# Performance work log

Hardware: AMD Instinct MI355X
Metric: run time of the kernel (lower is better)

Reference implementation:

```python
import jax, jax.numpy as jnp
import numpy as np

TAU = 0.95

def _f1_per_position(labels):
    # labels: [B, L] binary relevance. r[b, j] = F1 if the list is truncated at position j+1.
    B, L = labels.shape
    csum = jnp.cumsum(labels, axis=1)                       # [B, L] relevant docs kept at cutoff k=j+1
    k = jnp.arange(1, L + 1, dtype=labels.dtype)            # [L]
    total = jnp.sum(labels, axis=1, keepdims=True)          # [B, 1] total relevant per list
    prec = csum / k
    rec = jnp.where(total > 0, csum / jnp.maximum(total, 1.0), 0.0)
    denom = prec + rec
    return jnp.where(denom > 0, 2.0 * prec * rec / jnp.maximum(denom, 1e-20), 0.0)


def setup_inputs() -> dict:
    key = jax.random.key(0)
    k1, k2 = jax.random.split(key)
    B, L = 8192, 2048
    # output: per-position truncation probabilities in (0, 1); log() is applied in the loss.
    output = jax.random.uniform(k1, (B, L, 1), dtype=jnp.float32, minval=1e-4, maxval=1.0)
    labels = jax.random.randint(k2, (B, L), 0, 2).astype(jnp.float32)
    return {"output": output, "labels": labels}


def reference(output, labels):
    # output: [B, L, 1], labels: [B, L]
    B = output.shape[0]
    r = _f1_per_position(labels)                             # [B, L]
    # q = exp(r/tau) / sum_j exp(r/tau)  ==  softmax(r/tau) along positions
    q = jax.nn.softmax(r / TAU, axis=1)
    log_out = jnp.log(output[..., 0])                        # [B, L]
    return -jnp.sum(log_out * q) / B
```

## Files before the change

### kernel.cpp

```cpp
#include <hip/hip_runtime.h>


constexpr int L   = 2048;
constexpr int TPB = 256;
constexpr float TAU   = 0.95f;
constexpr float LOG2E = 1.4426950408889634f;
constexpr float LN2   = 0.6931471805599453f;

__global__ __launch_bounds__(TPB) void attncut_row_kernel(
    const float* __restrict__ output,
    const float* __restrict__ labels,
    float* __restrict__ rowloss,
    int B)
{
    const int wave = threadIdx.x >> 6;
    const int lane = threadIdx.x & 63;
    const int row  = blockIdx.x * 4 + wave;

    const float4* lab4 = reinterpret_cast<const float4*>(labels + (size_t)row * L) + lane;
    const float4* out4 = reinterpret_cast<const float4*>(output + (size_t)row * L) + lane;

    float4 lb[8], ov[8];
#pragma unroll
    for (int c = 0; c < 8; ++c) lb[c] = lab4[c * 64];
#pragma unroll
    for (int c = 0; c < 8; ++c) ov[c] = out4[c * 64];

    unsigned nibs = 0u;
#pragma unroll
    for (int c = 0; c < 8; ++c) {
        float4 a = lb[c];
        unsigned b = (unsigned)a.x | ((unsigned)a.y << 1)
                   | ((unsigned)a.z << 2) | ((unsigned)a.w << 3);
        nibs |= b << (4 * c);
    }

    unsigned w[4];
#pragma unroll
    for (int q = 0; q < 4; ++q) {
        unsigned c0 = __popc((nibs >> (8 * q)) & 0xFu);
        unsigned c1 = __popc((nibs >> (8 * q + 4)) & 0xFu);
        w[q] = c0 | (c1 << 16);
    }

#pragma unroll
    for (int d = 1; d < 64; d <<= 1) {
#pragma unroll
        for (int q = 0; q < 4; ++q) {
            unsigned n = __shfl_up(w[q], d, 64);
            if (lane >= d) w[q] += n;
        }
    }

    float T[8], E[8];
#pragma unroll
    for (int q = 0; q < 4; ++q) {
        unsigned tw = __shfl(w[q], 63, 64);
        unsigned own0 = __popc((nibs >> (8 * q)) & 0xFu);
        unsigned own1 = __popc((nibs >> (8 * q + 4)) & 0xFu);
        T[2 * q]     = (float)(tw & 0xFFFFu);
        T[2 * q + 1] = (float)(tw >> 16);
        E[2 * q]     = (float)((w[q] & 0xFFFFu) - own0);
        E[2 * q + 1] = (float)((w[q] >> 16) - own1);
    }
    const float total = ((T[0] + T[1]) + (T[2] + T[3])) + ((T[4] + T[5]) + (T[6] + T[7]));

    const float K2 = (total > 0.f) ? (2.f * LOG2E / TAU) : 0.f;

    float Z = 0.f, Wd = 0.f;
    float off = 0.f;
#pragma unroll
    for (int c = 0; c < 8; ++c) {
        float4 o = ov[c];
        float cf = off + E[c];
        const unsigned nib = (nibs >> (4 * c)) & 0xFu;
        const float kb = total + (float)(c * 256 + 4 * lane);

        cf += (float)(nib & 1u);
        float e0 = __builtin_amdgcn_exp2f((K2 * cf) * __builtin_amdgcn_rcpf(kb + 1.f));
        Z += e0;  Wd = fmaf(__builtin_amdgcn_logf(o.x), e0, Wd);

        cf += (float)((nib >> 1) & 1u);
        float e1 = __builtin_amdgcn_exp2f((K2 * cf) * __builtin_amdgcn_rcpf(kb + 2.f));
        Z += e1;  Wd = fmaf(__builtin_amdgcn_logf(o.y), e1, Wd);

        cf += (float)((nib >> 2) & 1u);
        float e2 = __builtin_amdgcn_exp2f((K2 * cf) * __builtin_amdgcn_rcpf(kb + 3.f));
        Z += e2;  Wd = fmaf(__builtin_amdgcn_logf(o.z), e2, Wd);

        cf += (float)((nib >> 3) & 1u);
        float e3 = __builtin_amdgcn_exp2f((K2 * cf) * __builtin_amdgcn_rcpf(kb + 4.f));
        Z += e3;  Wd = fmaf(__builtin_amdgcn_logf(o.w), e3, Wd);

        off += T[c];
    }

#pragma unroll
    for (int d = 32; d; d >>= 1) {
        Z  += __shfl_xor(Z, d, 64);
        Wd += __shfl_xor(Wd, d, 64);
    }
    if (lane == 0) rowloss[row] = -LN2 * Wd / Z;
}

__global__ __launch_bounds__(1024) void attncut_reduce_kernel(
    const float* __restrict__ rowloss, float* __restrict__ out, int B)
{
    const int t = threadIdx.x;
    const float4* r4 = reinterpret_cast<const float4*>(rowloss);
    float s = 0.f;
    for (int i = t; i < B / 4; i += 1024) {
        float4 v = r4[i];
        s += (v.x + v.y) + (v.z + v.w);
    }
#pragma unroll
    for (int d = 32; d; d >>= 1) s += __shfl_xor(s, d, 64);
    __shared__ float ws[16];
    if ((t & 63) == 0) ws[t >> 6] = s;
    __syncthreads();
    if (t < 16) {
        s = ws[t];
#pragma unroll
        for (int d = 8; d; d >>= 1) s += __shfl_xor(s, d, 64);
        if (t == 0) out[0] = s / (float)B;
    }
}

extern "C" void kernel_launch(void* const* d_in, const int* in_sizes, int n_in,
                              void* d_out, int out_size, void* d_ws, size_t ws_size,
                              hipStream_t stream) {
    const float* output = (const float*)d_in[0];
    const float* labels = (const float*)d_in[1];
    const int B = in_sizes[1] / L;

    float* rowloss = (float*)d_ws;

    attncut_row_kernel<<<B / 4, TPB, 0, stream>>>(output, labels, rowloss, B);
    attncut_reduce_kernel<<<1, 1024, 0, stream>>>(rowloss, (float*)d_out, B);
}
```

Before: 28.18 us.

## Process four rows per wave with double-buffered inline-asm prefetch pipeline

```diff
diff --git a/kernel.cpp b/kernel.cpp
--- a/kernel.cpp
+++ b/kernel.cpp
@@ -3,11 +3,110 @@
 
 constexpr int L   = 2048;
 constexpr int TPB = 256;
+constexpr int RPW = 4;
 constexpr float TAU   = 0.95f;
 constexpr float LOG2E = 1.4426950408889634f;
 constexpr float LN2   = 0.6931471805599453f;
 
-__global__ __launch_bounds__(TPB) void attncut_row_kernel(
+typedef float f32x4 __attribute__((ext_vector_type(4)));
+
+#define ISSUE8(buf, p) do {                                                              \
+    const f32x4* _p0 = (p);                                                              \
+    const f32x4* _p4 = (p) + 256;                                                        \
+    asm volatile("global_load_dwordx4 %0, %1, off"             : "=v"(buf[0]) : "v"(_p0)); \
+    asm volatile("global_load_dwordx4 %0, %1, off offset:1024" : "=v"(buf[1]) : "v"(_p0)); \
+    asm volatile("global_load_dwordx4 %0, %1, off offset:2048" : "=v"(buf[2]) : "v"(_p0)); \
+    asm volatile("global_load_dwordx4 %0, %1, off offset:3072" : "=v"(buf[3]) : "v"(_p0)); \
+    asm volatile("global_load_dwordx4 %0, %1, off"             : "=v"(buf[4]) : "v"(_p4)); \
+    asm volatile("global_load_dwordx4 %0, %1, off offset:1024" : "=v"(buf[5]) : "v"(_p4)); \
+    asm volatile("global_load_dwordx4 %0, %1, off offset:2048" : "=v"(buf[6]) : "v"(_p4)); \
+    asm volatile("global_load_dwordx4 %0, %1, off offset:3072" : "=v"(buf[7]) : "v"(_p4)); \
+} while (0)
+
+#define WAITV(n) do { asm volatile("s_waitcnt vmcnt(" #n ")");                           \
+                      __builtin_amdgcn_sched_barrier(0); } while (0)
+
+struct SS {
+    unsigned nibs;
+    float total, K2;
+    float T[8], E[8];
+};
+
+__device__ __forceinline__ SS do_scan(const f32x4 lb[8], int lane) {
+    SS s;
+    unsigned nibs = 0u;
+#pragma unroll
+    for (int c = 0; c < 8; ++c) {
+        unsigned b = (unsigned)lb[c][0] | ((unsigned)lb[c][1] << 1)
+                   | ((unsigned)lb[c][2] << 2) | ((unsigned)lb[c][3] << 3);
+        nibs |= b << (4 * c);
+    }
+    unsigned w[4];
+#pragma unroll
+    for (int q = 0; q < 4; ++q) {
+        unsigned c0 = __popc((nibs >> (8 * q)) & 0xFu);
+        unsigned c1 = __popc((nibs >> (8 * q + 4)) & 0xFu);
+        w[q] = c0 | (c1 << 16);
+    }
+#pragma unroll
+    for (int d = 1; d < 64; d <<= 1) {
+#pragma unroll
+        for (int q = 0; q < 4; ++q) {
+            unsigned n = __shfl_up(w[q], d, 64);
+            if (lane >= d) w[q] += n;
+        }
+    }
+#pragma unroll
+    for (int q = 0; q < 4; ++q) {
+        unsigned tw = __shfl(w[q], 63, 64);
+        unsigned own0 = __popc((nibs >> (8 * q)) & 0xFu);
+        unsigned own1 = __popc((nibs >> (8 * q + 4)) & 0xFu);
+        s.T[2 * q]     = (float)(tw & 0xFFFFu);
+        s.T[2 * q + 1] = (float)(tw >> 16);
+        s.E[2 * q]     = (float)((w[q] & 0xFFFFu) - own0);
+        s.E[2 * q + 1] = (float)((w[q] >> 16) - own1);
+    }
+    s.total = ((s.T[0] + s.T[1]) + (s.T[2] + s.T[3])) + ((s.T[4] + s.T[5]) + (s.T[6] + s.T[7]));
+    s.K2    = (s.total > 0.f) ? (2.f * LOG2E / TAU) : 0.f;
+    s.nibs  = nibs;
+    return s;
+}
+
+__device__ __forceinline__ float do_main(const f32x4 ov[8], const SS& s, int lane) {
+    float Z = 0.f, Wd = 0.f, off = 0.f;
+#pragma unroll
+    for (int c = 0; c < 8; ++c) {
+        float cf = off + s.E[c];
+        const unsigned nib = (s.nibs >> (4 * c)) & 0xFu;
+        const float kb = s.total + (float)(c * 256 + 4 * lane);
+
+        cf += (float)(nib & 1u);
+        float e0 = __builtin_amdgcn_exp2f((s.K2 * cf) * __builtin_amdgcn_rcpf(kb + 1.f));
+        Z += e0;  Wd = fmaf(__builtin_amdgcn_logf(ov[c][0]), e0, Wd);
+
+        cf += (float)((nib >> 1) & 1u);
+        float e1 = __builtin_amdgcn_exp2f((s.K2 * cf) * __builtin_amdgcn_rcpf(kb + 2.f));
+        Z += e1;  Wd = fmaf(__builtin_amdgcn_logf(ov[c][1]), e1, Wd);
+
+        cf += (float)((nib >> 2) & 1u);
+        float e2 = __builtin_amdgcn_exp2f((s.K2 * cf) * __builtin_amdgcn_rcpf(kb + 3.f));
+        Z += e2;  Wd = fmaf(__builtin_amdgcn_logf(ov[c][2]), e2, Wd);
+
+        cf += (float)((nib >> 3) & 1u);
+        float e3 = __builtin_amdgcn_exp2f((s.K2 * cf) * __builtin_amdgcn_rcpf(kb + 4.f));
+        Z += e3;  Wd = fmaf(__builtin_amdgcn_logf(ov[c][3]), e3, Wd);
+
+        off += s.T[c];
+    }
+#pragma unroll
+    for (int d = 32; d; d >>= 1) {
+        Z  += __shfl_xor(Z, d, 64);
+        Wd += __shfl_xor(Wd, d, 64);
+    }
+    return -LN2 * Wd / Z;
+}
+
+__global__ __launch_bounds__(TPB, 2) void attncut_row_kernel(
     const float* __restrict__ output,
     const float* __restrict__ labels,
     float* __restrict__ rowloss,
@@ -15,92 +114,54 @@
 {
     const int wave = threadIdx.x >> 6;
     const int lane = threadIdx.x & 63;
-    const int row  = blockIdx.x * 4 + wave;
-
-    const float4* lab4 = reinterpret_cast<const float4*>(labels + (size_t)row * L) + lane;
-    const float4* out4 = reinterpret_cast<const float4*>(output + (size_t)row * L) + lane;
-
-    float4 lb[8], ov[8];
-#pragma unroll
-    for (int c = 0; c < 8; ++c) lb[c] = lab4[c * 64];
-#pragma unroll
-    for (int c = 0; c < 8; ++c) ov[c] = out4[c * 64];
-
-    unsigned nibs = 0u;
-#pragma unroll
-    for (int c = 0; c < 8; ++c) {
-        float4 a = lb[c];
-        unsigned b = (unsigned)a.x | ((unsigned)a.y << 1)
-                   | ((unsigned)a.z << 2) | ((unsigned)a.w << 3);
-        nibs |= b << (4 * c);
-    }
-
-    unsigned w[4];
-#pragma unroll
-    for (int q = 0; q < 4; ++q) {
-        unsigned c0 = __popc((nibs >> (8 * q)) & 0xFu);
-        unsigned c1 = __popc((nibs >> (8 * q + 4)) & 0xFu);
-        w[q] = c0 | (c1 << 16);
-    }
-
-#pragma unroll
-    for (int d = 1; d < 64; d <<= 1) {
-#pragma unroll
-        for (int q = 0; q < 4; ++q) {
-            unsigned n = __shfl_up(w[q], d, 64);
-            if (lane >= d) w[q] += n;
-        }
-    }
-
-    float T[8], E[8];
-#pragma unroll
-    for (int q = 0; q < 4; ++q) {
-        unsigned tw = __shfl(w[q], 63, 64);
-        unsigned own0 = __popc((nibs >> (8 * q)) & 0xFu);
-        unsigned own1 = __popc((nibs >> (8 * q + 4)) & 0xFu);
-        T[2 * q]     = (float)(tw & 0xFFFFu);
-        T[2 * q + 1] = (float)(tw >> 16);
-        E[2 * q]     = (float)((w[q] & 0xFFFFu) - own0);
-        E[2 * q + 1] = (float)((w[q] >> 16) - own1);
-    }
-    const float total = ((T[0] + T[1]) + (T[2] + T[3])) + ((T[4] + T[5]) + (T[6] + T[7]));
-
-    const float K2 = (total > 0.f) ? (2.f * LOG2E / TAU) : 0.f;
-
-    float Z = 0.f, Wd = 0.f;
-    float off = 0.f;
-#pragma unroll
-    for (int c = 0; c < 8; ++c) {
-        float4 o = ov[c];
-        float cf = off + E[c];
-        const unsigned nib = (nibs >> (4 * c)) & 0xFu;
-        const float kb = total + (float)(c * 256 + 4 * lane);
-
-        cf += (float)(nib & 1u);
-        float e0 = __builtin_amdgcn_exp2f((K2 * cf) * __builtin_amdgcn_rcpf(kb + 1.f));
-        Z += e0;  Wd = fmaf(__builtin_amdgcn_logf(o.x), e0, Wd);
-
-        cf += (float)((nib >> 1) & 1u);
-        float e1 = __builtin_amdgcn_exp2f((K2 * cf) * __builtin_amdgcn_rcpf(kb + 2.f));
-        Z += e1;  Wd = fmaf(__builtin_amdgcn_logf(o.y), e1, Wd);
-
-        cf += (float)((nib >> 2) & 1u);
-        float e2 = __builtin_amdgcn_exp2f((K2 * cf) * __builtin_amdgcn_rcpf(kb + 3.f));
-        Z += e2;  Wd = fmaf(__builtin_amdgcn_logf(o.z), e2, Wd);
-
-        cf += (float)((nib >> 3) & 1u);
-        float e3 = __builtin_amdgcn_exp2f((K2 * cf) * __builtin_amdgcn_rcpf(kb + 4.f));
-        Z += e3;  Wd = fmaf(__builtin_amdgcn_logf(o.w), e3, Wd);
-
-        off += T[c];
-    }
-
-#pragma unroll
-    for (int d = 32; d; d >>= 1) {
-        Z  += __shfl_xor(Z, d, 64);
-        Wd += __shfl_xor(Wd, d, 64);
-    }
-    if (lane == 0) rowloss[row] = -LN2 * Wd / Z;
+    const int g    = blockIdx.x * 4 + wave;
+    const int row0 = g * RPW;
+
+    const f32x4* lp = reinterpret_cast<const f32x4*>(labels + (size_t)row0 * L) + lane;
+    const f32x4* op = reinterpret_cast<const f32x4*>(output + (size_t)row0 * L) + lane;
+
+    f32x4 Plb[8], Pov[8], Qlb[8], Qov[8];
+
+    ISSUE8(Plb, lp);
+    ISSUE8(Pov, op);
+
+    ISSUE8(Qlb, lp + 512);
+    WAITV(16);
+    SS s0 = do_scan(Plb, lane);
+    ISSUE8(Qov, op + 512);
+    WAITV(16);
+    {
+        float rl = do_main(Pov, s0, lane);
+        if (lane == 0) rowloss[row0 + 0] = rl;
+    }
+
+    ISSUE8(Plb, lp + 1024);
+    WAITV(16);
+    SS s1 = do_scan(Qlb, lane);
+    ISSUE8(Pov, op + 1024);
+    WAITV(16);
+    {
+        float rl = do_main(Qov, s1, lane);
+        if (lane == 0) rowloss[row0 + 1] = rl;
+    }
+
+    ISSUE8(Qlb, lp + 1536);
+    WAITV(16);
+    SS s2 = do_scan(Plb, lane);
+    ISSUE8(Qov, op + 1536);
+    WAITV(16);
+    {
+        float rl = do_main(Pov, s2, lane);
+        if (lane == 0) rowloss[row0 + 2] = rl;
+    }
+
+    WAITV(8);
+    SS s3 = do_scan(Qlb, lane);
+    WAITV(0);
+    {
+        float rl = do_main(Qov, s3, lane);
+        if (lane == 0) rowloss[row0 + 3] = rl;
+    }
 }
 
 __global__ __launch_bounds__(1024) void attncut_reduce_kernel(
@@ -135,6 +196,7 @@
 
     float* rowloss = (float*)d_ws;
 
-    attncut_row_kernel<<<B / 4, TPB, 0, stream>>>(output, labels, rowloss, B);
+    const int blocks = B / (4 * RPW);
+    attncut_row_kernel<<<blocks, TPB, 0, stream>>>(output, labels, rowloss, B);
     attncut_reduce_kernel<<<1, 1024, 0, stream>>>(rowloss, (float*)d_out, B);
 }
```

New measurement: 29.57 us. +4.9%, slower.
